# Kernel optimization log

Hardware: AMD Instinct MI355X
Metric: run time of the kernel (lower is better)

Reference implementation:

```python
import jax, jax.numpy as jnp
import numpy as np

N, E = 16384, 65536
N2, A2, E2 = 65536, 131072, 262144
N3, A3, E3 = 65536, 196608, 262144
B = 256
F_IN, NI2, NI3 = 16, 64, 64


def setup_inputs() -> dict:
    key = jax.random.key(0)
    ks = iter(jax.random.split(key, 80))
    def rn(shape, s=1.0):
        return jax.random.normal(next(ks), shape, jnp.float32) * s
    def ru(shape):
        return jax.random.uniform(next(ks), shape, dtype=jnp.float32)
    def ri(shape, hi):
        return jax.random.randint(next(ks), shape, 0, hi)
    s = 0.05
    inp = {
        "x": rn((N, F_IN)),
        "edge_index": ri((2, E), N),
        "edge_attr": ru((E, 7)),
        "batch": jnp.sort(ri((N,), B)),
        "assign2_node": ri((A2,), N),
        "assign2_cluster": ri((A2,), N2),
        "iso_type_2": ru((N2, NI2)),
        "edge_index_2": ri((2, E2), N2),
        "batch_2": jnp.sort(ri((N2,), B)),
        "assign3_node": ri((A3,), N),
        "assign3_cluster": ri((A3,), N3),
        "iso_type_3": ru((N3, NI3)),
        "edge_index_3": ri((2, E3), N3),
        "batch_3": jnp.sort(ri((N3,), B)),
    }
    for i, (mi, mo) in enumerate([(F_IN, 32), (32, 64), (64, 64)], start=1):
        inp[f"nn{i}_W1"] = rn((7, 128), s)
        inp[f"nn{i}_b1"] = jnp.zeros((128,), jnp.float32)
        inp[f"nn{i}_W2"] = rn((128, mi * mo), s)
        inp[f"nn{i}_b2"] = jnp.zeros((mi * mo,), jnp.float32)
        inp[f"conv{i}_root"] = rn((mi, mo), s)
        inp[f"conv{i}_bias"] = jnp.zeros((mo,), jnp.float32)
    for i, din in zip([4, 5, 6, 7], [64 + NI2, 64, 64 + NI3, 64]):
        inp[f"conv{i}_Wrel"] = rn((din, 64), s)
        inp[f"conv{i}_Wroot"] = rn((din, 64), s)
        inp[f"conv{i}_bias"] = jnp.zeros((64,), jnp.float32)
    inp["fc1_W"] = rn((384, 64), s); inp["fc1_b"] = jnp.zeros((64,), jnp.float32)
    inp["fc2_W"] = rn((64, 32), s); inp["fc2_b"] = jnp.zeros((32,), jnp.float32)
    inp["fc3_W"] = rn((32, 1), s); inp["fc3_b"] = jnp.zeros((1,), jnp.float32)
    return inp


def nnconv(x, ei, ea, W1, b1, W2, b2, root, bias, mi, mo):
    # edge MLP -> per-edge [mi, mo] weight matrix; message = x_src @ W_e; scatter-add to dst
    h = jax.nn.relu(ea @ W1 + b1) @ W2 + b2          # [E, mi*mo]
    We = h.reshape(-1, mi, mo)
    msg = jnp.einsum('ei,eio->eo', x[ei[0]], We)     # [E, mo]
    agg = jax.ops.segment_sum(msg, ei[1], num_segments=x.shape[0])
    return x @ root + agg + bias


def graphconv(x, ei, Wrel, Wroot, bias):
    agg = jax.ops.segment_sum(x[ei[0]], ei[1], num_segments=x.shape[0])
    return agg @ Wrel + x @ Wroot + bias


def avg_pool_assign(x, node_idx, cluster_idx, num_clusters):
    s = jax.ops.segment_sum(x[node_idx], cluster_idx, num_segments=num_clusters)
    c = jax.ops.segment_sum(jnp.ones((node_idx.shape[0],), x.dtype), cluster_idx, num_segments=num_clusters)
    return s / jnp.clip(c, 1.0)[:, None]


def reference(x, edge_index, edge_attr, batch, assign2_node, assign2_cluster, iso_type_2, edge_index_2, batch_2, assign3_node, assign3_cluster, iso_type_3, edge_index_3, batch_3, nn1_W1, nn1_b1, nn1_W2, nn1_b2, conv1_root, conv1_bias, nn2_W1, nn2_b1, nn2_W2, nn2_b2, conv2_root, conv2_bias, nn3_W1, nn3_b1, nn3_W2, nn3_b2, conv3_root, conv3_bias, conv4_Wrel, conv4_Wroot, conv4_bias, conv5_Wrel, conv5_Wroot, conv5_bias, conv6_Wrel, conv6_Wroot, conv6_bias, conv7_Wrel, conv7_Wroot, conv7_bias, fc1_W, fc1_b, fc2_W, fc2_b, fc3_W, fc3_b):
    elu = jax.nn.elu
    h = elu(nnconv(x, edge_index, edge_attr, nn1_W1, nn1_b1, nn1_W2, nn1_b2, conv1_root, conv1_bias, F_IN, 32))
    h = elu(nnconv(h, edge_index, edge_attr, nn2_W1, nn2_b1, nn2_W2, nn2_b2, conv2_root, conv2_bias, 32, 64))
    h = elu(nnconv(h, edge_index, edge_attr, nn3_W1, nn3_b1, nn3_W2, nn3_b2, conv3_root, conv3_bias, 64, 64))
    x_1 = jax.ops.segment_sum(h, batch, num_segments=B)
    # 2-set level
    h2 = avg_pool_assign(h, assign2_node, assign2_cluster, N2)
    h2 = jnp.concatenate([h2, iso_type_2], axis=1)
    h2 = elu(graphconv(h2, edge_index_2, conv4_Wrel, conv4_Wroot, conv4_bias))
    h2 = elu(graphconv(h2, edge_index_2, conv5_Wrel, conv5_Wroot, conv5_bias))
    x_2 = jax.ops.segment_sum(h2, batch_2, num_segments=B)
    # 3-set level
    h3 = avg_pool_assign(h, assign3_node, assign3_cluster, N3)
    h3 = jnp.concatenate([h3, iso_type_3], axis=1)
    h3 = elu(graphconv(h3, edge_index_3, conv6_Wrel, conv6_Wroot, conv6_bias))
    h3 = elu(graphconv(h3, edge_index_3, conv7_Wrel, conv7_Wroot, conv7_bias))
    x_3 = jax.ops.segment_sum(h3, batch_3, num_segments=B)
    xc = jnp.concatenate([x_1, x_2, x_3], axis=1)
    xc = jnp.concatenate([xc, xc], axis=1)      # [B, 384]
    o = elu(xc @ fc1_W + fc1_b)
    o = elu(o @ fc2_W + fc2_b)
    o = o @ fc3_W + fc3_b
    return o.reshape(-1)
```

## Files before the change

kernel.cpp:

```cpp
#include <hip/hip_runtime.h>
#include <math.h>

#define NN 16384
#define E1N 65536
#define NBATCH 256
#define NC2 65536
#define KH 128
#define OCSTR 136
#define NSTR 1096

typedef _Float16 f16;
typedef _Float16 f16x2 __attribute__((ext_vector_type(2)));
typedef _Float16 f16x8 __attribute__((ext_vector_type(8)));
typedef float    f32x4 __attribute__((ext_vector_type(4)));

__device__ __forceinline__ float elu1(float x){ return x > 0.f ? x : expm1f(x); }

__device__ __forceinline__ float dot2acc(f16x2 a, f16x2 b, float c){
#if __has_builtin(__builtin_amdgcn_fdot2)
  return __builtin_amdgcn_fdot2(a, b, c, false);
#else
  return fmaf((float)a[0], (float)b[0], fmaf((float)a[1], (float)b[1], c));
#endif
}

__global__ __launch_bounds__(256) void k_count(const int* __restrict__ arr, int* __restrict__ cnt, int n){
  int i = blockIdx.x*256 + threadIdx.x;
  if (i < n) atomicAdd(&cnt[arr[i]], 1);
}

__global__ __launch_bounds__(256) void k_scan1(const int* __restrict__ deg,
    int* __restrict__ ptr, int* __restrict__ partials){
  __shared__ int buf[256];
  int i = blockIdx.x*256 + threadIdx.x, t = threadIdx.x;
  int v = deg[i];
  buf[t] = v; __syncthreads();
  for (int o = 1; o < 256; o <<= 1){
    int x = (t >= o) ? buf[t-o] : 0;
    __syncthreads(); buf[t] += x; __syncthreads();
  }
  ptr[i] = buf[t] - v;
  if (t == 255) partials[blockIdx.x] = buf[255];
}

__global__ __launch_bounds__(256) void k_scan2(int* __restrict__ partials, int nb){
  __shared__ int buf[256];
  int t = threadIdx.x;
  int v = (t < nb) ? partials[t] : 0;
  buf[t] = v; __syncthreads();
  for (int o = 1; o < 256; o <<= 1){
    int x = (t >= o) ? buf[t-o] : 0;
    __syncthreads(); buf[t] += x; __syncthreads();
  }
  if (t < nb) partials[t] = buf[t] - v;
}

__global__ __launch_bounds__(256) void k_scan3(const int* __restrict__ partials,
    int* __restrict__ ptr, int* __restrict__ cur){
  int i = blockIdx.x*256 + threadIdx.x;
  int v = ptr[i] + partials[blockIdx.x];
  ptr[i] = v; cur[i] = v;
}

__global__ __launch_bounds__(256) void k_fill_edge(const int* __restrict__ ei, int* __restrict__ cursor,
    int* __restrict__ eids, int* __restrict__ srcs, int* __restrict__ dsts){
  int e = blockIdx.x*256 + threadIdx.x;
  if (e >= E1N) return;
  int s = ei[e];
  int p = atomicAdd(&cursor[s], 1);
  eids[p] = e; srcs[p] = s; dsts[p] = ei[E1N + e];
}

__global__ __launch_bounds__(256) void k_fill_dst(const int* __restrict__ eiL, int* __restrict__ cur,
    int* __restrict__ dsrc, int EL){
  int e = blockIdx.x*256 + threadIdx.x;
  if (e >= EL) return;
  int d = eiL[EL + e];
  int p = atomicAdd(&cur[d], 1);
  dsrc[p] = eiL[e];
}

__global__ __launch_bounds__(256) void k_fill_assign(const int* __restrict__ an, const int* __restrict__ ac,
    int* __restrict__ cur, int* __restrict__ an_sorted, int A){
  int a = blockIdx.x*256 + threadIdx.x;
  if (a >= A) return;
  int c = ac[a];
  int p = atomicAdd(&cur[c], 1);
  an_sorted[p] = an[a];
}

__global__ __launch_bounds__(256) void k_cvt16(const float* __restrict__ v, f16* __restrict__ o, int n){
  int t = blockIdx.x*256 + threadIdx.x;
  if (t < n) o[t] = (f16)v[t];
}

__global__ __launch_bounds__(256) void k_elu_both(float* __restrict__ v, f16* __restrict__ v16, int n){
  int t = blockIdx.x*256 + threadIdx.x;
  if (t < n){ float r = elu1(v[t]); v[t] = r; v16[t] = (f16)r; }
}

__global__ __launch_bounds__(256) void k_elu(float* __restrict__ v, int n){
  int t = blockIdx.x*256 + threadIdx.x;
  if (t < n) v[t] = elu1(v[t]);
}

__global__ __launch_bounds__(256) void k_edge_mlp(const float* __restrict__ ea,
    const int* __restrict__ eids,
    const float* __restrict__ W1, const float* __restrict__ b1,
    f16* __restrict__ hrelu){
  int t = blockIdx.x*256 + threadIdx.x;
  if (t >= E1N*KH) return;
  int p = t >> 7, k = t & 127;
  const float* row = ea + (size_t)eids[p]*7;
  float acc = b1[k];
  #pragma unroll
  for (int i=0;i<7;i++) acc = fmaf(row[i], W1[i*KH+k], acc);
  hrelu[t] = (f16)fmaxf(acc, 0.f);
}

__global__ __launch_bounds__(256) void k_packPrep(const float* __restrict__ root,
    const float* __restrict__ b2, f16* __restrict__ Bp, int mi, int mo, int S, int NB){
  int t = blockIdx.x*256 + threadIdx.x;
  if (t >= NB*S*512) return;
  int j = t & 7, l = (t >> 3) & 63, cs = t >> 9;
  int s = cs % S, c = cs / S;
  int k_in = s*32 + ((l>>4)<<3) + j;
  int n = c*16 + (l & 15);
  float v = 0.f;
  if (k_in < mi) v = (n < mo) ? root[k_in*mo + n] : b2[k_in*mo + (n - mo)];
  Bp[t] = (f16)v;
}

template<int MI, int S, int NB, int MO>
__global__ __launch_bounds__(256) void k_prep_mfma(const f16* __restrict__ A,
    const f16* __restrict__ Bp, const float* __restrict__ bias,
    float* __restrict__ outb, float* __restrict__ bterm){
  int l = threadIdx.x & 63, w = threadIdx.x >> 6;
  int r0 = blockIdx.x*64 + w*16;
  const f16* arow = A + (size_t)(r0 + (l & 15))*MI;
  f16x8 a[S];
  #pragma unroll
  for (int s=0;s<S;s++){
    int koff = s*32 + ((l>>4)<<3);
    if (koff < MI) a[s] = *(const f16x8*)(arow + koff);
    else           a[s] = (f16x8){0,0,0,0,0,0,0,0};
  }
  #pragma unroll
  for (int c=0;c<NB;c++){
    f32x4 acc = (f32x4){0.f,0.f,0.f,0.f};
    #pragma unroll
    for (int s=0;s<S;s++){
      f16x8 b = *(const f16x8*)(Bp + ((size_t)(c*S + s)*64 + l)*8);
      acc = __builtin_amdgcn_mfma_f32_16x16x32_f16(a[s], b, acc, 0, 0, 0);
    }
    int col = c*16 + (l & 15);
    #pragma unroll
    for (int r=0;r<4;r++){
      int row = r0 + ((l>>4)<<2) + r;
      if (col < MO) outb[(size_t)row*MO + col] = acc[r] + bias[col];
      else          bterm[(size_t)row*MO + (col - MO)] = acc[r];
    }
  }
}

__global__ __launch_bounds__(256) void k_w2pack_full(const float* __restrict__ W2,
    f16* __restrict__ Bp, int mi, int mo, int S){
  int t = blockIdx.x*256 + threadIdx.x;
  if (t >= mo*8*S*512) return;
  int j = t & 7, l = (t >> 3) & 63, cs = t >> 9;
  int s = cs % S, q = cs / S;
  int oc = q >> 3;
  int k  = (q & 7)*16 + (l & 15);
  int i  = s*32 + ((l>>4)<<3) + j;
  float v = (i < mi) ? W2[(size_t)k*mi*mo + (size_t)i*mo + oc] : 0.f;
  Bp[t] = (f16)v;
}

template<int MI, int S, int MO>
__global__ __launch_bounds__(256) void k_nnconv_fused(const f16* __restrict__ xin16,
    const f16* __restrict__ W2p,
    const int* __restrict__ rowptr, const int* __restrict__ rowend,
    const int* __restrict__ srcs, const int* __restrict__ dsts,
    const f16* __restrict__ hrelu, const float* __restrict__ bterm,
    float* __restrict__ outb){
  __shared__ __align__(16) f16 M[16*NSTR];
  int l = threadIdx.x & 63, w = threadIdx.x >> 6;
  int n0 = blockIdx.x * 16;
  int estart = rowptr[n0];
  int eend   = rowend[n0 + 15];
  if (estart >= eend) return;
  const f16* arow = xin16 + (size_t)(n0 + (l & 15))*MI;
  f16x8 a[S];
  #pragma unroll
  for (int s=0;s<S;s++){
    int koff = s*32 + ((l>>4)<<3);
    if (koff < MI) a[s] = *(const f16x8*)(arow + koff);
    else           a[s] = (f16x8){0,0,0,0,0,0,0,0};
  }
  int eslot = l >> 3, oc = l & 7;
  int passes = (eend - estart + 31) >> 5;
  const int NCHUNK = MO/8;
  for (int c = 0; c < NCHUNK; c++){
    #pragma unroll
    for (int t=0;t<16;t++){
      int q = c*64 + w*16 + t;
      f32x4 acc = (f32x4){0.f,0.f,0.f,0.f};
      #pragma unroll
      for (int s=0;s<S;s++){
        f16x8 b = *(const f16x8*)(W2p + ((size_t)(q*S + s)*64 + l)*8);
        acc = __builtin_amdgcn_mfma_f32_16x16x32_f16(a[s], b, acc, 0, 0, 0);
      }
      int ocl = w*2 + (t>>3);
      int k0  = (t&7)*16 + (l & 15);
      f16* mp = &M[ocl*OCSTR + k0];
      #pragma unroll
      for (int r=0;r<4;r++)
        mp[(size_t)(((l>>4)<<2) + r)*NSTR] = (f16)acc[r];
    }
    __syncthreads();
    for (int p = 0; p < passes; p++){
      int e = estart + p*32 + w*8 + eslot;
      if (e < eend){
        int s_ = srcs[e];
        int ln = s_ - n0;
        float acc = bterm[(size_t)s_*MO + c*8 + oc];
        const f16x8* hr = (const f16x8*)(hrelu + (size_t)e*KH);
        const f16* mrow = &M[(size_t)ln*NSTR + oc*OCSTR];
        #pragma unroll 4
        for (int kk=0; kk<16; kk++){
          f16x8 h8 = hr[kk];
          f16x8 m8 = *(const f16x8*)(mrow + kk*8);
          #pragma unroll
          for (int j=0;j<4;j++){
            f16x2 hp = {h8[2*j], h8[2*j+1]};
            f16x2 mp2 = {m8[2*j], m8[2*j+1]};
            acc = dot2acc(hp, mp2, acc);
          }
        }
        atomicAdd(&outb[(size_t)dsts[e]*MO + c*8 + oc], acc);
      }
    }
    __syncthreads();
  }
}

__global__ __launch_bounds__(256) void k_pool_gather(const int* __restrict__ aptr,
    const int* __restrict__ aend, const int* __restrict__ an_sorted,
    const float* __restrict__ h, const float* __restrict__ iso,
    f16* __restrict__ h16){
  int l = threadIdx.x & 63, w = threadIdx.x >> 6;
  int c = blockIdx.x*4 + w;
  int st = aptr[c], en = aend[c];
  float acc = 0.f;
  int e = st;
  for (; e+1 < en; e += 2){
    int n0 = an_sorted[e], n1 = an_sorted[e+1];
    acc += h[(size_t)n0*64 + l];
    acc += h[(size_t)n1*64 + l];
  }
  if (e < en) acc += h[(size_t)an_sorted[e]*64 + l];
  int cnt = en - st;
  float val = (cnt > 0) ? acc / (float)cnt : 0.f;
  h16[(size_t)c*128 + l] = (f16)val;
  h16[(size_t)c*128 + 64 + l] = (f16)iso[(size_t)c*64 + l];
}

__global__ __launch_bounds__(256) void k_packB_gc(const float* __restrict__ Wrel,
    const float* __restrict__ Wroot, f16* __restrict__ Bp, int S){
  int t = blockIdx.x*256 + threadIdx.x;
  if (t >= 8*S*512) return;
  int j = t & 7, l = (t >> 3) & 63, cs = t >> 9;
  int s = cs % S, c = cs / S;
  int k = s*32 + ((l>>4)<<3) + j;
  int n = (c<<4) + (l & 15);
  float v = (n < 64) ? Wrel[k*64 + n] : Wroot[k*64 + (n - 64)];
  Bp[t] = (f16)v;
}

template<int S>
__global__ __launch_bounds__(256) void k_gc_mfma(const f16* __restrict__ A,
    const f16* __restrict__ Bp, const float* __restrict__ bias,
    float* __restrict__ y, float* __restrict__ rbuf){
  int l = threadIdx.x & 63, w = threadIdx.x >> 6;
  int r0 = blockIdx.x*64 + w*16;
  const f16* arow = A + (size_t)(r0 + (l & 15))*(S*32);
  f16x8 a[S];
  #pragma unroll
  for (int s=0;s<S;s++) a[s] = *(const f16x8*)(arow + s*32 + ((l>>4)<<3));
  f32x4 acc[8];
  #pragma unroll
  for (int c=0;c<8;c++) acc[c] = (f32x4){0.f,0.f,0.f,0.f};
  #pragma unroll
  for (int c=0;c<8;c++){
    #pragma unroll
    for (int s=0;s<S;s++){
      f16x8 b = *(const f16x8*)(Bp + ((size_t)(c*S + s)*64 + l)*8);
      acc[c] = __builtin_amdgcn_mfma_f32_16x16x32_f16(a[s], b, acc[c], 0, 0, 0);
    }
  }
  #pragma unroll
  for (int c=0;c<8;c++){
    int col = c*16 + (l & 15);
    #pragma unroll
    for (int r=0;r<4;r++){
      int row = r0 + ((l>>4)<<2) + r;
      if (col < 64) y[(size_t)row*64 + col] = acc[c][r];
      else          rbuf[(size_t)row*64 + (col-64)] = acc[c][r] + bias[col-64];
    }
  }
}

template<bool F16OUT>
__global__ __launch_bounds__(256) void k_gc_gather(const int* __restrict__ dptr,
    const int* __restrict__ dend, const int* __restrict__ dsrc,
    const float* __restrict__ y, const float* __restrict__ rbuf,
    f16* __restrict__ o16, float* __restrict__ o32){
  int l = threadIdx.x & 63, w = threadIdx.x >> 6;
  int n = blockIdx.x*4 + w;
  int st = dptr[n], en = dend[n];
  float acc = rbuf[(size_t)n*64 + l];
  int e = st;
  for (; e+1 < en; e += 2){
    int s0 = dsrc[e], s1 = dsrc[e+1];
    acc += y[(size_t)s0*64 + l];
    acc += y[(size_t)s1*64 + l];
  }
  if (e < en) acc += y[(size_t)dsrc[e]*64 + l];
  float r = elu1(acc);
  if (F16OUT) o16[(size_t)n*64 + l] = (f16)r;
  else        o32[(size_t)n*64 + l] = r;
}

__device__ __forceinline__ int lowerb(const int* __restrict__ a, int n, int key){
  int lo = 0, hi = n;
  while (lo < hi){ int m = (lo + hi) >> 1; if (a[m] < key) lo = m + 1; else hi = m; }
  return lo;
}

__global__ __launch_bounds__(256) void k_batchsum_seg(const int* __restrict__ batch,
    const float* __restrict__ h, float* __restrict__ x123, int n_nodes, int off){
  __shared__ float red[4][64];
  int b = blockIdx.x;
  int lo = lowerb(batch, n_nodes, b);
  int hi = lowerb(batch, n_nodes, b+1);
  int col = threadIdx.x & 63, wq = threadIdx.x >> 6;
  float acc = 0.f;
  for (int n = lo + wq; n < hi; n += 4) acc += h[(size_t)n*64 + col];
  red[wq][col] = acc;
  __syncthreads();
  if (threadIdx.x < 64){
    float s = red[0][threadIdx.x] + red[1][threadIdx.x] + red[2][threadIdx.x] + red[3][threadIdx.x];
    x123[b*192 + off + threadIdx.x] = s;
  }
}

__global__ __launch_bounds__(256) void k_fc1(const float* __restrict__ x123,
    const float* __restrict__ W, const float* __restrict__ b, float* __restrict__ t1){
  int t = blockIdx.x*256 + threadIdx.x;
  if (t >= NBATCH*64) return;
  int bb = t >> 6, o = t & 63;
  const float* xr = x123 + bb*192;
  float acc = b[o];
  for (int j=0;j<192;j++) acc = fmaf(xr[j], W[j*64+o] + W[(192+j)*64+o], acc);
  t1[t] = elu1(acc);
}

__global__ __launch_bounds__(256) void k_fc2(const float* __restrict__ t1,
    const float* __restrict__ W, const float* __restrict__ b, float* __restrict__ t2){
  int t = blockIdx.x*256 + threadIdx.x;
  if (t >= NBATCH*32) return;
  int bb = t >> 5, o = t & 31;
  float acc = b[o];
  for (int j=0;j<64;j++) acc = fmaf(t1[bb*64+j], W[j*32+o], acc);
  t2[t] = elu1(acc);
}

__global__ __launch_bounds__(256) void k_fc3(const float* __restrict__ t2,
    const float* __restrict__ W, const float* __restrict__ b, float* __restrict__ out){
  int t = blockIdx.x*256 + threadIdx.x;
  if (t >= NBATCH) return;
  float acc = b[0];
  for (int j=0;j<32;j++) acc = fmaf(t2[t*32+j], W[j], acc);
  out[t] = acc;
}

static inline int cdiv(long long a, int b){ return (int)((a + b - 1) / b); }

extern "C" void kernel_launch(void* const* d_in, const int* in_sizes, int n_in,
                              void* d_out, int out_size, void* d_ws, size_t ws_size,
                              hipStream_t stream) {
  const float* x0    = (const float*)d_in[0];
  const int*   ei    = (const int*)d_in[1];
  const float* ea    = (const float*)d_in[2];
  const int*   batch = (const int*)d_in[3];
  const int*   a2n   = (const int*)d_in[4];
  const int*   a2c   = (const int*)d_in[5];
  const float* iso2  = (const float*)d_in[6];
  const int*   ei2   = (const int*)d_in[7];
  const int*   b2arr = (const int*)d_in[8];
  const int*   a3n   = (const int*)d_in[9];
  const int*   a3c   = (const int*)d_in[10];
  const float* iso3  = (const float*)d_in[11];
  const int*   ei3   = (const int*)d_in[12];
  const int*   b3arr = (const int*)d_in[13];
  const float* nnp[3][6];
  for (int c=0;c<3;c++) for (int p=0;p<6;p++) nnp[c][p] = (const float*)d_in[14 + 6*c + p];
  const float* c4W[3]; const float* c5W[3]; const float* c6W[3]; const float* c7W[3];
  for (int p=0;p<3;p++){ c4W[p]=(const float*)d_in[32+p]; c5W[p]=(const float*)d_in[35+p];
                         c6W[p]=(const float*)d_in[38+p]; c7W[p]=(const float*)d_in[41+p]; }
  const float* fc1W=(const float*)d_in[44]; const float* fc1b=(const float*)d_in[45];
  const float* fc2W=(const float*)d_in[46]; const float* fc2b=(const float*)d_in[47];
  const float* fc3W=(const float*)d_in[48]; const float* fc3b=(const float*)d_in[49];
  float* outp = (float*)d_out;

  char* ws = (char*)d_ws; size_t off = 0;
  auto alloc = [&](size_t bytes)->void*{ void* p = ws + off; off += (bytes + 255) & ~(size_t)255; return p; };
  const size_t SZ_R0 = (size_t)92*1024*1024;
  char* r0 = (char*)alloc(SZ_R0);
  f16*   hrelu = (f16*)r0;
  f16*   W2p   = (f16*)(r0 + (size_t)E1N*KH*2);
  f16*   prepB = (f16*)(r0 + (size_t)E1N*KH*2 + 2*1024*1024);
  float* bterm = (float*)(r0 + (size_t)E1N*KH*2 + 2*1024*1024 + 64*1024);
  size_t o2 = 0;
  auto a2 = [&](size_t bytes)->char*{ char* p = r0 + o2; o2 += (bytes + 255) & ~(size_t)255; return p; };
  f16*   h16   = (f16*)  a2((size_t)NC2*128*2);
  float* ybuf  = (float*)a2((size_t)NC2*64*4);
  float* rbuf  = (float*)a2((size_t)NC2*64*4);
  float* gB    = (float*)a2((size_t)NC2*64*4);
  f16*   g16   = (f16*)  a2((size_t)NC2*64*2);
  f16*   BpGc  = (f16*)  a2((size_t)8*4*512*2);
  int*   aptr  = (int*)  a2((size_t)NC2*4);
  int*   acur  = (int*)  a2((size_t)NC2*4);
  int*   dptr  = (int*)  a2((size_t)NC2*4);
  int*   dcur  = (int*)  a2((size_t)NC2*4);
  int*   ldeg  = (int*)  a2((size_t)NC2*4);
  int*   ans   = (int*)  a2((size_t)196608*4);
  int*   dsrc  = (int*)  a2((size_t)262144*4);
  float* hA    = (float*)alloc((size_t)NN*32*4);
  float* hB    = (float*)alloc((size_t)NN*64*4);
  float* hC    = (float*)alloc((size_t)NN*64*4);
  f16*   x016  = (f16*)  alloc((size_t)NN*16*2);
  f16*   hA16  = (f16*)  alloc((size_t)NN*32*2);
  f16*   hB16  = (f16*)  alloc((size_t)NN*64*2);
  int*   deg   = (int*)  alloc((size_t)NN*4);
  int*   cursor= (int*)  alloc((size_t)NN*4);
  int*   rowptr= (int*)  alloc((size_t)NN*4);
  int*   eids  = (int*)  alloc((size_t)E1N*4);
  int*   srcs  = (int*)  alloc((size_t)E1N*4);
  int*   dsts  = (int*)  alloc((size_t)E1N*4);
  int*   parts = (int*)  alloc((size_t)256*4);
  float* x123  = (float*)alloc((size_t)NBATCH*192*4);
  float* t1    = (float*)alloc((size_t)NBATCH*64*4);
  float* t2    = (float*)alloc((size_t)NBATCH*32*4);
  (void)ws_size; (void)n_in; (void)in_sizes; (void)out_size;

  auto scan = [&](const int* dg, int n, int* ptr, int* cur){
    k_scan1<<<n/256,256,0,stream>>>(dg, ptr, parts);
    k_scan2<<<1,256,0,stream>>>(parts, n/256);
    k_scan3<<<n/256,256,0,stream>>>(parts, ptr, cur);
  };

  hipMemsetAsync(deg, 0, (size_t)NN*4, stream);
  k_count<<<cdiv(E1N,256),256,0,stream>>>(ei, deg, E1N);
  scan(deg, NN, rowptr, cursor);
  k_fill_edge<<<cdiv(E1N,256),256,0,stream>>>(ei, cursor, eids, srcs, dsts);
  k_cvt16<<<cdiv((long long)NN*16,256),256,0,stream>>>(x0, x016, NN*16);

  auto run_nnconv = [&](const f16* xin16, int mi, int mo,
                        const float* const* P, float* outb, f16* out16){
    const float* W1=P[0]; const float* b1=P[1]; const float* W2=P[2];
    const float* b2=P[3]; const float* root=P[4]; const float* bias=P[5];
    const int S = (mi > 32) ? 2 : 1;
    const int NB = (2*mo)/16;
    k_edge_mlp<<<cdiv((long long)E1N*KH,256),256,0,stream>>>(ea, eids, W1, b1, hrelu);
    k_packPrep<<<cdiv((long long)NB*S*512,256),256,0,stream>>>(root, b2, prepB, mi, mo, S, NB);
    if (mi==16)      k_prep_mfma<16,1,4,32><<<NN/64,256,0,stream>>>(xin16, prepB, bias, outb, bterm);
    else if (mi==32) k_prep_mfma<32,1,8,64><<<NN/64,256,0,stream>>>(xin16, prepB, bias, outb, bterm);
    else             k_prep_mfma<64,2,8,64><<<NN/64,256,0,stream>>>(xin16, prepB, bias, outb, bterm);
    k_w2pack_full<<<cdiv((long long)mo*8*S*512,256),256,0,stream>>>(W2, W2p, mi, mo, S);
    if (mi==16)      k_nnconv_fused<16,1,32><<<NN/16,256,0,stream>>>(xin16, W2p, rowptr, cursor, srcs, dsts, hrelu, bterm, outb);
    else if (mi==32) k_nnconv_fused<32,1,64><<<NN/16,256,0,stream>>>(xin16, W2p, rowptr, cursor, srcs, dsts, hrelu, bterm, outb);
    else             k_nnconv_fused<64,2,64><<<NN/16,256,0,stream>>>(xin16, W2p, rowptr, cursor, srcs, dsts, hrelu, bterm, outb);
    if (out16) k_elu_both<<<cdiv((long long)NN*mo,256),256,0,stream>>>(outb, out16, NN*mo);
    else       k_elu<<<cdiv((long long)NN*mo,256),256,0,stream>>>(outb, NN*mo);
  };
  run_nnconv(x016, 16, 32, nnp[0], hA, hA16);
  run_nnconv(hA16, 32, 64, nnp[1], hB, hB16);
  run_nnconv(hB16, 64, 64, nnp[2], hC, nullptr);

  k_batchsum_seg<<<NBATCH,256,0,stream>>>(batch, hC, x123, NN, 0);

  auto run_level = [&](const int* an, const int* ac, int A, const float* iso,
                       const int* eiL, int EL, const int* batchL,
                       const float* const* cA, const float* const* cB, int off123){
    hipMemsetAsync(ldeg, 0, (size_t)NC2*4, stream);
    k_count<<<cdiv(A,256),256,0,stream>>>(ac, ldeg, A);
    scan(ldeg, NC2, aptr, acur);
    k_fill_assign<<<cdiv(A,256),256,0,stream>>>(an, ac, acur, ans, A);
    hipMemsetAsync(ldeg, 0, (size_t)NC2*4, stream);
    k_count<<<cdiv(EL,256),256,0,stream>>>(eiL + EL, ldeg, EL);
    scan(ldeg, NC2, dptr, dcur);
    k_fill_dst<<<cdiv(EL,256),256,0,stream>>>(eiL, dcur, dsrc, EL);
    k_pool_gather<<<NC2/4,256,0,stream>>>(aptr, acur, ans, hC, iso, h16);
    k_packB_gc<<<cdiv((long long)8*4*512,256),256,0,stream>>>(cA[0], cA[1], BpGc, 4);
    k_gc_mfma<4><<<NC2/64,256,0,stream>>>(h16, BpGc, cA[2], ybuf, rbuf);
    k_gc_gather<true><<<NC2/4,256,0,stream>>>(dptr, dcur, dsrc, ybuf, rbuf, g16, nullptr);
    k_packB_gc<<<cdiv((long long)8*2*512,256),256,0,stream>>>(cB[0], cB[1], BpGc, 2);
    k_gc_mfma<2><<<NC2/64,256,0,stream>>>(g16, BpGc, cB[2], ybuf, rbuf);
    k_gc_gather<false><<<NC2/4,256,0,stream>>>(dptr, dcur, dsrc, ybuf, rbuf, nullptr, gB);
    k_batchsum_seg<<<NBATCH,256,0,stream>>>(batchL, gB, x123, NC2, off123);
  };
  run_level(a2n, a2c, 131072, iso2, ei2, 262144, b2arr, c4W, c5W, 64);
  run_level(a3n, a3c, 196608, iso3, ei3, 262144, b3arr, c6W, c7W, 128);

  k_fc1<<<cdiv((long long)NBATCH*64,256),256,0,stream>>>(x123, fc1W, fc1b, t1);
  k_fc2<<<cdiv((long long)NBATCH*32,256),256,0,stream>>>(t1, fc2W, fc2b, t2);
  k_fc3<<<cdiv(NBATCH,256),256,0,stream>>>(t2, fc3W, fc3b, outp);
}
```

Before: 899.4 us.

## Fuse edge MLP into NNConv kernel with single-wave blocks over edge tiles

```diff
diff --git a/kernel.cpp b/kernel.cpp
--- a/kernel.cpp
+++ b/kernel.cpp
@@ -7,10 +7,12 @@
 #define NC2 65536
 #define KH 128
 #define OCSTR 136
-#define NSTR 1096
+#define NSTR4 1096
+#define ETILE 16
 
 typedef _Float16 f16;
 typedef _Float16 f16x2 __attribute__((ext_vector_type(2)));
+typedef _Float16 f16x4 __attribute__((ext_vector_type(4)));
 typedef _Float16 f16x8 __attribute__((ext_vector_type(8)));
 typedef float    f32x4 __attribute__((ext_vector_type(4)));
 
@@ -104,20 +106,6 @@
   if (t < n) v[t] = elu1(v[t]);
 }
 
-__global__ __launch_bounds__(256) void k_edge_mlp(const float* __restrict__ ea,
-    const int* __restrict__ eids,
-    const float* __restrict__ W1, const float* __restrict__ b1,
-    f16* __restrict__ hrelu){
-  int t = blockIdx.x*256 + threadIdx.x;
-  if (t >= E1N*KH) return;
-  int p = t >> 7, k = t & 127;
-  const float* row = ea + (size_t)eids[p]*7;
-  float acc = b1[k];
-  #pragma unroll
-  for (int i=0;i<7;i++) acc = fmaf(row[i], W1[i*KH+k], acc);
-  hrelu[t] = (f16)fmaxf(acc, 0.f);
-}
-
 __global__ __launch_bounds__(256) void k_packPrep(const float* __restrict__ root,
     const float* __restrict__ b2, f16* __restrict__ Bp, int mi, int mo, int S, int NB){
   int t = blockIdx.x*256 + threadIdx.x;
@@ -177,19 +165,23 @@
 }
 
 template<int MI, int S, int MO>
-__global__ __launch_bounds__(256) void k_nnconv_fused(const f16* __restrict__ xin16,
+__global__ __launch_bounds__(64) void k_nnconv_fused2(const f16* __restrict__ xin16,
     const f16* __restrict__ W2p,
     const int* __restrict__ rowptr, const int* __restrict__ rowend,
     const int* __restrict__ srcs, const int* __restrict__ dsts,
-    const f16* __restrict__ hrelu, const float* __restrict__ bterm,
-    float* __restrict__ outb){
-  __shared__ __align__(16) f16 M[16*NSTR];
-  int l = threadIdx.x & 63, w = threadIdx.x >> 6;
-  int n0 = blockIdx.x * 16;
-  int estart = rowptr[n0];
-  int eend   = rowend[n0 + 15];
+    const int* __restrict__ eids,
+    const float* __restrict__ ea, const float* __restrict__ W1,
+    const float* __restrict__ b1,
+    const float* __restrict__ bterm, float* __restrict__ outb){
+  __shared__ __align__(16) f16  M[4*NSTR4];
+  __shared__ __align__(16) f16  hb[ETILE*OCSTR];
+  __shared__ __align__(16) float eas[ETILE*8];
+  int l = threadIdx.x;
+  int n0 = blockIdx.x*4;
+  int estart = rowptr[n0], eend = rowend[n0+3];
   if (estart >= eend) return;
-  const f16* arow = xin16 + (size_t)(n0 + (l & 15))*MI;
+  int an = n0 + (((l&15) < 4) ? (l&15) : 3);
+  const f16* arow = xin16 + (size_t)an*MI;
   f16x8 a[S];
   #pragma unroll
   for (int s=0;s<S;s++){
@@ -197,50 +189,85 @@
     if (koff < MI) a[s] = *(const f16x8*)(arow + koff);
     else           a[s] = (f16x8){0,0,0,0,0,0,0,0};
   }
+  const int NCHUNK = MO/8;
   int eslot = l >> 3, oc = l & 7;
-  int passes = (eend - estart + 31) >> 5;
-  const int NCHUNK = MO/8;
-  for (int c = 0; c < NCHUNK; c++){
-    #pragma unroll
-    for (int t=0;t<16;t++){
-      int q = c*64 + w*16 + t;
-      f32x4 acc = (f32x4){0.f,0.f,0.f,0.f};
+  for (int ebase = estart; ebase < eend; ebase += ETILE){
+    int ecnt = eend - ebase; if (ecnt > ETILE) ecnt = ETILE;
+    for (int idx = l; idx < ecnt*8; idx += 64){
+      int e_ = idx >> 3, i = idx & 7;
+      eas[idx] = (i < 7) ? ea[(size_t)eids[ebase + e_]*7 + i] : 0.f;
+    }
+    __asm__ volatile("s_waitcnt vmcnt(0) lgkmcnt(0)" ::: "memory");
+    {
+      int e_ = l & 15, kg = l >> 4;
+      if (e_ < ecnt){
+        float xr[7];
+        #pragma unroll
+        for (int i=0;i<7;i++) xr[i] = eas[e_*8 + i];
+        #pragma unroll 2
+        for (int jj = 0; jj < 32; jj += 4){
+          int k0 = kg*32 + jj;
+          float4 acc4 = *(const float4*)(b1 + k0);
+          #pragma unroll
+          for (int i=0;i<7;i++){
+            float4 wv = *(const float4*)(W1 + i*KH + k0);
+            acc4.x = fmaf(xr[i], wv.x, acc4.x);
+            acc4.y = fmaf(xr[i], wv.y, acc4.y);
+            acc4.z = fmaf(xr[i], wv.z, acc4.z);
+            acc4.w = fmaf(xr[i], wv.w, acc4.w);
+          }
+          f16x4 hv = { (f16)fmaxf(acc4.x,0.f), (f16)fmaxf(acc4.y,0.f),
+                       (f16)fmaxf(acc4.z,0.f), (f16)fmaxf(acc4.w,0.f) };
+          *(f16x4*)&hb[e_*OCSTR + k0] = hv;
+        }
+      }
+    }
+    __asm__ volatile("s_waitcnt vmcnt(0) lgkmcnt(0)" ::: "memory");
+    for (int c = 0; c < NCHUNK; c++){
+      #pragma unroll 8
+      for (int t = 0; t < 64; t++){
+        int q = c*64 + t;
+        f32x4 acc = (f32x4){0.f,0.f,0.f,0.f};
+        #pragma unroll
+        for (int s=0;s<S;s++){
+          f16x8 b = *(const f16x8*)(W2p + ((size_t)(q*S + s)*64 + l)*8);
+          acc = __builtin_amdgcn_mfma_f32_16x16x32_f16(a[s], b, acc, 0, 0, 0);
+        }
+        if ((l >> 4) == 0){
+          int ocl = t >> 3, kpos = (t & 7)*16 + (l & 15);
+          f16* mp = &M[ocl*OCSTR + kpos];
+          #pragma unroll
+          for (int r=0;r<4;r++)
+            mp[(size_t)r*NSTR4] = (f16)acc[r];
+        }
+      }
+      __asm__ volatile("s_waitcnt lgkmcnt(0)" ::: "memory");
       #pragma unroll
-      for (int s=0;s<S;s++){
-        f16x8 b = *(const f16x8*)(W2p + ((size_t)(q*S + s)*64 + l)*8);
-        acc = __builtin_amdgcn_mfma_f32_16x16x32_f16(a[s], b, acc, 0, 0, 0);
+      for (int r2 = 0; r2 < 2; r2++){
+        int ee = r2*8 + eslot;
+        if (ee < ecnt){
+          int e = ebase + ee;
+          int s_ = srcs[e];
+          int ln = s_ - n0;
+          float acc = bterm[(size_t)s_*MO + c*8 + oc];
+          const f16* mrow = &M[(size_t)ln*NSTR4 + oc*OCSTR];
+          const f16* hrow = &hb[ee*OCSTR];
+          #pragma unroll 4
+          for (int kk=0; kk<16; kk++){
+            f16x8 m8 = *(const f16x8*)(mrow + kk*8);
+            f16x8 h8 = *(const f16x8*)(hrow + kk*8);
+            #pragma unroll
+            for (int j=0;j<4;j++){
+              f16x2 hp = {h8[2*j], h8[2*j+1]};
+              f16x2 mp2 = {m8[2*j], m8[2*j+1]};
+              acc = dot2acc(hp, mp2, acc);
+            }
+          }
+          atomicAdd(&outb[(size_t)dsts[e]*MO + c*8 + oc], acc);
+        }
       }
-      int ocl = w*2 + (t>>3);
-      int k0  = (t&7)*16 + (l & 15);
-      f16* mp = &M[ocl*OCSTR + k0];
-      #pragma unroll
-      for (int r=0;r<4;r++)
-        mp[(size_t)(((l>>4)<<2) + r)*NSTR] = (f16)acc[r];
-    }
-    __syncthreads();
-    for (int p = 0; p < passes; p++){
-      int e = estart + p*32 + w*8 + eslot;
-      if (e < eend){
-        int s_ = srcs[e];
-        int ln = s_ - n0;
-        float acc = bterm[(size_t)s_*MO + c*8 + oc];
-        const f16x8* hr = (const f16x8*)(hrelu + (size_t)e*KH);
-        const f16* mrow = &M[(size_t)ln*NSTR + oc*OCSTR];
-        #pragma unroll 4
-        for (int kk=0; kk<16; kk++){
-          f16x8 h8 = hr[kk];
-          f16x8 m8 = *(const f16x8*)(mrow + kk*8);
-          #pragma unroll
-          for (int j=0;j<4;j++){
-            f16x2 hp = {h8[2*j], h8[2*j+1]};
-            f16x2 mp2 = {m8[2*j], m8[2*j+1]};
-            acc = dot2acc(hp, mp2, acc);
-          }
-        }
-        atomicAdd(&outb[(size_t)dsts[e]*MO + c*8 + oc], acc);
-      }
-    }
-    __syncthreads();
+      __asm__ volatile("s_waitcnt lgkmcnt(0)" ::: "memory");
+    }
   }
 }
 
@@ -417,10 +444,9 @@
   auto alloc = [&](size_t bytes)->void*{ void* p = ws + off; off += (bytes + 255) & ~(size_t)255; return p; };
   const size_t SZ_R0 = (size_t)92*1024*1024;
   char* r0 = (char*)alloc(SZ_R0);
-  f16*   hrelu = (f16*)r0;
-  f16*   W2p   = (f16*)(r0 + (size_t)E1N*KH*2);
-  f16*   prepB = (f16*)(r0 + (size_t)E1N*KH*2 + 2*1024*1024);
-  float* bterm = (float*)(r0 + (size_t)E1N*KH*2 + 2*1024*1024 + 64*1024);
+  f16*   W2p   = (f16*)r0;
+  f16*   prepB = (f16*)(r0 + 2*1024*1024);
+  float* bterm = (float*)(r0 + 2*1024*1024 + 64*1024);
   size_t o2 = 0;
   auto a2 = [&](size_t bytes)->char*{ char* p = r0 + o2; o2 += (bytes + 255) & ~(size_t)255; return p; };
   f16*   h16   = (f16*)  a2((size_t)NC2*128*2);
@@ -472,15 +498,14 @@
     const float* b2=P[3]; const float* root=P[4]; const float* bias=P[5];
     const int S = (mi > 32) ? 2 : 1;
     const int NB = (2*mo)/16;
-    k_edge_mlp<<<cdiv((long long)E1N*KH,256),256,0,stream>>>(ea, eids, W1, b1, hrelu);
     k_packPrep<<<cdiv((long long)NB*S*512,256),256,0,stream>>>(root, b2, prepB, mi, mo, S, NB);
     if (mi==16)      k_prep_mfma<16,1,4,32><<<NN/64,256,0,stream>>>(xin16, prepB, bias, outb, bterm);
     else if (mi==32) k_prep_mfma<32,1,8,64><<<NN/64,256,0,stream>>>(xin16, prepB, bias, outb, bterm);
     else             k_prep_mfma<64,2,8,64><<<NN/64,256,0,stream>>>(xin16, prepB, bias, outb, bterm);
     k_w2pack_full<<<cdiv((long long)mo*8*S*512,256),256,0,stream>>>(W2, W2p, mi, mo, S);
-    if (mi==16)      k_nnconv_fused<16,1,32><<<NN/16,256,0,stream>>>(xin16, W2p, rowptr, cursor, srcs, dsts, hrelu, bterm, outb);
-    else if (mi==32) k_nnconv_fused<32,1,64><<<NN/16,256,0,stream>>>(xin16, W2p, rowptr, cursor, srcs, dsts, hrelu, bterm, outb);
-    else             k_nnconv_fused<64,2,64><<<NN/16,256,0,stream>>>(xin16, W2p, rowptr, cursor, srcs, dsts, hrelu, bterm, outb);
+    if (mi==16)      k_nnconv_fused2<16,1,32><<<NN/4,64,0,stream>>>(xin16, W2p, rowptr, cursor, srcs, dsts, eids, ea, W1, b1, bterm, outb);
+    else if (mi==32) k_nnconv_fused2<32,1,64><<<NN/4,64,0,stream>>>(xin16, W2p, rowptr, cursor, srcs, dsts, eids, ea, W1, b1, bterm, outb);
+    else             k_nnconv_fused2<64,2,64><<<NN/4,64,0,stream>>>(xin16, W2p, rowptr, cursor, srcs, dsts, eids, ea, W1, b1, bterm, outb);
     if (out16) k_elu_both<<<cdiv((long long)NN*mo,256),256,0,stream>>>(outb, out16, NN*mo);
     else       k_elu<<<cdiv((long long)NN*mo,256),256,0,stream>>>(outb, NN*mo);
   };
```

Result: slower. 1.767 ms (+96.4%).
